# Optimization experiments

Hardware: AMD Instinct MI355X
Metric: run time of the kernel (lower is better)

The kernel has to match this reference:

```python
import jax, jax.numpy as jnp
import numpy as np

HEAD_SIZE = 64


def setup_inputs() -> dict:
    key = jax.random.key(0)
    kx, kq, kk, kv = jax.random.split(key, 4)
    B, L, D = 4, 4096, 1024
    scale = 1.0 / np.sqrt(D)
    x = jax.random.normal(kx, (B, L, D), dtype=jnp.float32)
    Wq = jax.random.normal(kq, (D, HEAD_SIZE), dtype=jnp.float32) * scale
    Wk = jax.random.normal(kk, (D, HEAD_SIZE), dtype=jnp.float32) * scale
    Wv = jax.random.normal(kv, (D, HEAD_SIZE), dtype=jnp.float32) * scale
    return {"x": x, "Wq": Wq, "Wk": Wk, "Wv": Wv}


def reference(x, Wq, Wk, Wv):
    B, L, D = x.shape
    H = Wq.shape[1]
    q = jnp.einsum('bld,dh->blh', x, Wq)  # [B,L,H]
    k = jnp.einsum('bld,dh->blh', x, Wk)
    v = jnp.einsum('bld,dh->blh', x, Wv)
    # full L x L score matrix, as in the original module
    scores = jnp.einsum('bqh,bkh->bqk', q, k) / jnp.sqrt(jnp.float32(H))
    causal = jnp.tril(jnp.ones((L, L), dtype=bool))
    scores = jnp.where(causal, scores, -jnp.inf)
    attn = jax.nn.softmax(scores, axis=-1)
    z = jnp.einsum('bqk,bkh->bqh', attn, v)  # [B,L,H]
    return z
```

## Files before the change

kernel.cpp:

```cpp
#include <hip/hip_runtime.h>
#include <stdint.h>

#define L_SEQ 4096
#define D_MODEL 1024
#define HEAD 64
#define CHUNK 512
#define MAXCH 8

typedef unsigned short u16;
typedef __attribute__((ext_vector_type(8))) short bf16x8;
typedef __attribute__((ext_vector_type(4))) float f32x4;

static __device__ __forceinline__ u16 f2bf(float f) {
    union { float f; uint32_t u; } c; c.f = f;
    uint32_t u = c.u;
    return (u16)((u + 0x7FFFu + ((u >> 16) & 1u)) >> 16);
}
static __device__ __forceinline__ bf16x8 ld8(const u16* p) { return *(const bf16x8*)p; }

static __device__ __forceinline__ f32x4 mfma16(bf16x8 a, bf16x8 b, f32x4 c) {
    return __builtin_amdgcn_mfma_f32_16x16x32_bf16(a, b, c, 0, 0, 0);
}

__global__ __launch_bounds__(256) void conv_w(
    const float* __restrict__ Wq, const float* __restrict__ Wk,
    const float* __restrict__ Wv, u16* __restrict__ Wt)
{
    __shared__ u16 tile[64][72];
    const float* W = (blockIdx.y == 0) ? Wq : (blockIdx.y == 1) ? Wk : Wv;
    u16* dst = Wt + blockIdx.y * (HEAD * D_MODEL);
    const int k0 = blockIdx.x * 64, t = threadIdx.x;
    #pragma unroll
    for (int i = 0; i < 16; i++) {
        int idx = i * 256 + t;
        int kk = idx >> 6, h = idx & 63;
        tile[h][kk] = f2bf(W[(size_t)(k0 + kk) * HEAD + h]);
    }
    __syncthreads();
    #pragma unroll
    for (int i = 0; i < 16; i++) {
        int idx = i * 256 + t;
        int h = idx >> 6, kk = idx & 63;
        dst[(size_t)h * D_MODEL + k0 + kk] = tile[h][kk];
    }
}

__global__ __launch_bounds__(256) void qkv_proj(
    const float* __restrict__ x, const u16* __restrict__ Wt,
    u16* __restrict__ qb, u16* __restrict__ kb, u16* __restrict__ vTb)
{
    __shared__ __align__(16) char smem[64512];
    u16* WlB = (u16*)smem;
    u16* XlB = (u16*)(smem + 55296);
    u16* CtB = (u16*)smem;
#define WL(bb,r,c) WlB[((bb)*192 + (r))*72 + (c)]
#define XL(bb,r,c) XlB[((bb)*32  + (r))*72 + (c)]
#define CT(r,c)    CtB[(r)*200 + (c)]

    const int t = threadIdx.x;
    const int wv = t >> 6, lane = t & 63;
    const int ln16 = lane & 15, quad = lane >> 4;
    const int w3 = wv * 3;
    const int m0 = blockIdx.x * 32;

    f32x4 acc[2][3] = {};

    auto stage = [&](int s, int bb) {
        const int k0 = s * 64;
        #pragma unroll
        for (int i = 0; i < 6; i++) {
            int idx = i * 256 + t;
            int row = idx >> 3, cg = (idx & 7) * 8;
            bf16x8 wv8 = ld8(&Wt[(size_t)row * D_MODEL + k0 + cg]);
            *(bf16x8*)&WL(bb, row, cg) = wv8;
        }
        #pragma unroll
        for (int i = 0; i < 2; i++) {
            int idx = i * 256 + t;
            int row = idx >> 4, cs = (idx & 15) * 4;
            const float4 xv = *(const float4*)&x[(size_t)(m0 + row) * D_MODEL + k0 + cs];
            uint2 pk;
            pk.x = (uint32_t)f2bf(xv.x) | ((uint32_t)f2bf(xv.y) << 16);
            pk.y = (uint32_t)f2bf(xv.z) | ((uint32_t)f2bf(xv.w) << 16);
            *(uint2*)&XL(bb, row, cs) = pk;
        }
    };

    stage(0, 0);
    int buf = 0;
    for (int s = 0; s < 16; s++) {
        __syncthreads();
        if (s + 1 < 16) stage(s + 1, buf ^ 1);
        #pragma unroll
        for (int c = 0; c < 2; c++) {
            bf16x8 xb0 = ld8(&XL(buf, ln16,      c * 32 + quad * 8));
            bf16x8 xb1 = ld8(&XL(buf, 16 + ln16, c * 32 + quad * 8));
            #pragma unroll
            for (int j = 0; j < 3; j++) {
                bf16x8 af = ld8(&WL(buf, (w3 + j) * 16 + ln16, c * 32 + quad * 8));
                acc[0][j] = mfma16(af, xb0, acc[0][j]);
                acc[1][j] = mfma16(af, xb1, acc[1][j]);
            }
        }
        buf ^= 1;
    }

    __syncthreads();
    #pragma unroll
    for (int mt = 0; mt < 2; mt++) {
        #pragma unroll
        for (int j = 0; j < 3; j++) {
            int g0 = (w3 + j) * 16 + quad * 4;
            float sc = (g0 < 64) ? 0.125f : 1.0f;
            uint2 pk;
            pk.x = (uint32_t)f2bf(acc[mt][j][0] * sc) | ((uint32_t)f2bf(acc[mt][j][1] * sc) << 16);
            pk.y = (uint32_t)f2bf(acc[mt][j][2] * sc) | ((uint32_t)f2bf(acc[mt][j][3] * sc) << 16);
            *(uint2*)&CT(mt * 16 + ln16, g0) = pk;
        }
    }
    __syncthreads();
    {
        int m = t >> 3, hg = (t & 7) * 8;
        *(bf16x8*)&qb[(size_t)(m0 + m) * HEAD + hg] = *(bf16x8*)&CT(m, hg);
        *(bf16x8*)&kb[(size_t)(m0 + m) * HEAD + hg] = *(bf16x8*)&CT(m, 64 + hg);
        int h = t >> 2, mg = (t & 3) * 8;
        bf16x8 vv;
        #pragma unroll
        for (int jj = 0; jj < 8; jj++) vv[jj] = (short)CT(mg + jj, 128 + h);
        int bbt = m0 >> 12, l0 = m0 & 4095;
        *(bf16x8*)&vTb[(size_t)(bbt * HEAD + h) * L_SEQ + l0 + mg] = vv;
    }
#undef WL
#undef XL
#undef CT
}

__global__ __launch_bounds__(256) void attn_chunk(
    const u16* __restrict__ qb, const u16* __restrict__ kb,
    const u16* __restrict__ vT, float* __restrict__ Opart, float* __restrict__ lpart)
{
    const int qt = blockIdx.x, ch = blockIdx.y, b = blockIdx.z;
    if (ch * CHUNK > qt * 64 + 63) return;

    __shared__ __align__(16) char smem[18432];

    const int t = threadIdx.x, wv = t >> 6, lane = t & 63;
    const int ln16 = lane & 15, quad = lane >> 4;
    const int qh = wv & 1, kvh = wv >> 1;
    const int qmin0 = qt * 64 + qh * 32;

    u16 (*P)[72] = (u16(*)[72])smem + wv * 32;
    float (*Cb)[68] = (float(*)[68])smem;
    float* Lb = (float*)(smem + 17408);

    bf16x8 qf[2][2];
    #pragma unroll
    for (int qn = 0; qn < 2; qn++) {
        const u16* qrp = qb + (size_t)(b * L_SEQ + qmin0 + qn * 16 + ln16) * HEAD + quad * 8;
        qf[qn][0] = ld8(qrp); qf[qn][1] = ld8(qrp + 32);
    }

    const u16* kbb = kb + (size_t)b * L_SEQ * HEAD;
    const u16* vbb = vT + (size_t)b * HEAD * L_SEQ;

    f32x4 o[2][4] = {};
    float lsum[2] = {0.f, 0.f};

    const int kv_lo = ch * CHUNK + kvh * (CHUNK / 2);
    const int kv_hi = min(kv_lo + CHUNK / 2, qt * 64 + 64);

    bf16x8 kf0a, kf0b, kf1a, kf1b;
    if (kv_lo < kv_hi) {
        const u16* kr0 = kbb + (size_t)(kv_lo + ln16) * HEAD + quad * 8;
        kf0a = ld8(kr0); kf0b = ld8(kr0 + 32);
        const u16* kr1 = kbb + (size_t)(kv_lo + 16 + ln16) * HEAD + quad * 8;
        kf1a = ld8(kr1); kf1b = ld8(kr1 + 32);
    }

    for (int kv0 = kv_lo; kv0 < kv_hi; kv0 += 64) {
        const u16* kr2 = kbb + (size_t)(kv0 + 32 + ln16) * HEAD + quad * 8;
        bf16x8 kf2a = ld8(kr2), kf2b = ld8(kr2 + 32);
        const u16* kr3 = kbb + (size_t)(kv0 + 48 + ln16) * HEAD + quad * 8;
        bf16x8 kf3a = ld8(kr3), kf3b = ld8(kr3 + 32);
        int kv0n = (kv0 + 64 < kv_hi) ? kv0 + 64 : kv_lo;
        const u16* nr0 = kbb + (size_t)(kv0n + ln16) * HEAD + quad * 8;
        bf16x8 nk0a = ld8(nr0), nk0b = ld8(nr0 + 32);
        const u16* nr1 = kbb + (size_t)(kv0n + 16 + ln16) * HEAD + quad * 8;
        bf16x8 nk1a = ld8(nr1), nk1b = ld8(nr1 + 32);
        const u16* vr0 = vbb + (size_t)ln16 * L_SEQ + kv0 + quad * 8;
        bf16x8 vf0a = ld8(vr0), vf0b = ld8(vr0 + 32);
        const u16* vr1 = vbb + (size_t)(16 + ln16) * L_SEQ + kv0 + quad * 8;
        bf16x8 vf1a = ld8(vr1), vf1b = ld8(vr1 + 32);

        #pragma unroll
        for (int g = 0; g < 4; g++) {
            bf16x8 ka = (g == 0) ? kf0a : (g == 1) ? kf1a : (g == 2) ? kf2a : kf3a;
            bf16x8 kb8 = (g == 0) ? kf0b : (g == 1) ? kf1b : (g == 2) ? kf2b : kf3b;
            #pragma unroll
            for (int qn = 0; qn < 2; qn++) {
                f32x4 s = {};
                s = mfma16(ka, qf[qn][0], s);
                s = mfma16(kb8, qf[qn][1], s);
                float p0, p1, p2, p3;
                if (kv0 + g * 16 + 15 <= qmin0 + qn * 16) {
                    p0 = __expf(s[0]); p1 = __expf(s[1]);
                    p2 = __expf(s[2]); p3 = __expf(s[3]);
                } else {
                    int q = qmin0 + qn * 16 + ln16;
                    int kv = kv0 + g * 16 + quad * 4;
                    p0 = (kv     <= q) ? __expf(s[0]) : 0.f;
                    p1 = (kv + 1 <= q) ? __expf(s[1]) : 0.f;
                    p2 = (kv + 2 <= q) ? __expf(s[2]) : 0.f;
                    p3 = (kv + 3 <= q) ? __expf(s[3]) : 0.f;
                }
                lsum[qn] += p0 + p1 + p2 + p3;
                uint32_t lo = (uint32_t)f2bf(p0) | ((uint32_t)f2bf(p1) << 16);
                uint32_t hi = (uint32_t)f2bf(p2) | ((uint32_t)f2bf(p3) << 16);
                uint32_t* dst = (uint32_t*)&P[qn * 16 + ln16][g * 16 + quad * 4];
                dst[0] = lo; dst[1] = hi;
            }
        }
        bf16x8 pf0[2], pf1[2];
        #pragma unroll
        for (int qn = 0; qn < 2; qn++) {
            pf0[qn] = ld8(&P[qn * 16 + ln16][quad * 8]);
            pf1[qn] = ld8(&P[qn * 16 + ln16][32 + quad * 8]);
        }
        #pragma unroll
        for (int hg = 0; hg < 4; hg++) {
            bf16x8 va, vb2;
            if (hg == 0) { va = vf0a; vb2 = vf0b; }
            else if (hg == 1) { va = vf1a; vb2 = vf1b; }
            else {
                const u16* vr = vbb + (size_t)(hg * 16 + ln16) * L_SEQ + kv0 + quad * 8;
                va = ld8(vr); vb2 = ld8(vr + 32);
            }
            #pragma unroll
            for (int qn = 0; qn < 2; qn++) {
                o[qn][hg] = mfma16(va, pf0[qn], o[qn][hg]);
                o[qn][hg] = mfma16(vb2, pf1[qn], o[qn][hg]);
            }
        }
        kf0a = nk0a; kf0b = nk0b; kf1a = nk1a; kf1b = nk1b;
    }

    #pragma unroll
    for (int qn = 0; qn < 2; qn++) {
        lsum[qn] += __shfl_xor(lsum[qn], 16);
        lsum[qn] += __shfl_xor(lsum[qn], 32);
    }

    __syncthreads();
    if (kvh == 1) {
        #pragma unroll
        for (int qn = 0; qn < 2; qn++) {
            #pragma unroll
            for (int hg = 0; hg < 4; hg++)
                *(f32x4*)&Cb[qh * 32 + qn * 16 + ln16][hg * 16 + quad * 4] = o[qn][hg];
            if (quad == 0) Lb[qh * 32 + qn * 16 + ln16] = lsum[qn];
        }
    }
    __syncthreads();
    if (kvh == 0) {
        const size_t base = (size_t)((b * 64 + qt) * MAXCH + ch);
        #pragma unroll
        for (int qn = 0; qn < 2; qn++) {
            int qrow = qh * 32 + qn * 16 + ln16;
            #pragma unroll
            for (int hg = 0; hg < 4; hg++) {
                f32x4 other = *(f32x4*)&Cb[qrow][hg * 16 + quad * 4];
                f32x4 r = o[qn][hg];
                r[0] += other[0]; r[1] += other[1]; r[2] += other[2]; r[3] += other[3];
                *(f32x4*)&Opart[base * 4096 + (size_t)qrow * 64 + hg * 16 + quad * 4] = r;
            }
            if (quad == 0)
                lpart[base * 64 + qrow] = lsum[qn] + Lb[qrow];
        }
    }
}

__global__ __launch_bounds__(256) void merge_chunks(
    const float* __restrict__ Opart, const float* __restrict__ lpart,
    float* __restrict__ out)
{
    const int qt = blockIdx.x, b = blockIdx.y;
    const int nch = qt / 8 + 1;
    const int t = threadIdx.x;
    const size_t obase = (size_t)((b * 64 + qt) * MAXCH) * 4096;
    const size_t lbase = (size_t)((b * 64 + qt) * MAXCH) * 64;
    #pragma unroll
    for (int i = 0; i < 4; i++) {
        int idx = i * 256 + t;
        int q = idx >> 4, hg = (idx & 15) * 4;
        float L = 0.f;
        float ax = 0.f, ay = 0.f, az = 0.f, aw = 0.f;
        for (int c = 0; c < nch; c++) {
            L += lpart[lbase + c * 64 + q];
            const float4 v = *(const float4*)&Opart[obase + (size_t)c * 4096 + q * 64 + hg];
            ax += v.x; ay += v.y; az += v.z; aw += v.w;
        }
        float inv = 1.f / L;
        float4 r; r.x = ax * inv; r.y = ay * inv; r.z = az * inv; r.w = aw * inv;
        *(float4*)&out[((size_t)(b * L_SEQ + qt * 64 + q)) * HEAD + hg] = r;
    }
}

extern "C" void kernel_launch(void* const* d_in, const int* in_sizes, int n_in,
                              void* d_out, int out_size, void* d_ws, size_t ws_size,
                              hipStream_t stream) {
    const float* x  = (const float*)d_in[0];
    const float* Wq = (const float*)d_in[1];
    const float* Wk = (const float*)d_in[2];
    const float* Wv = (const float*)d_in[3];
    float* out = (float*)d_out;

    u16* ws16 = (u16*)d_ws;
    u16* Wt  = ws16;
    u16* qb  = Wt + 3 * HEAD * D_MODEL;
    u16* kb  = qb + 16384 * HEAD;
    u16* vTb = kb + 16384 * HEAD;
    float* Opart = (float*)(vTb + 16384 * HEAD);
    float* lpart = Opart + (size_t)2048 * 4096;

    conv_w      <<<dim3(16, 3), 256, 0, stream>>>(Wq, Wk, Wv, Wt);
    qkv_proj    <<<dim3(512), 256, 0, stream>>>(x, Wt, qb, kb, vTb);
    attn_chunk  <<<dim3(64, 8, 4), 256, 0, stream>>>(qb, kb, vTb, Opart, lpart);
    merge_chunks<<<dim3(64, 4), 256, 0, stream>>>(Opart, lpart, out);
}
```

Measured before the change: 175.5 us.

## Split attention into 32-row query tiles with four KV-split waves and preloaded K/V

Query tiles shrink from 64 to 32 rows, doubling the grid, and the four waves in a block now each take a 128-key slice of the chunk instead of a 2x2 query/KV split. All K and V fragments for a wave's two 64-key tiles are loaded up front, and the partial results are reduced across waves through shared memory. The merge kernel loads all chunk partials unconditionally and masks them. The aim is more blocks and better load balance across the causal triangle, plus more latency hiding from bulk loads, at the cost of higher register pressure, a larger LDS footprint and more partial-result traffic.

```diff
diff --git a/kernel.cpp b/kernel.cpp
--- a/kernel.cpp
+++ b/kernel.cpp
@@ -6,6 +6,7 @@
 #define HEAD 64
 #define CHUNK 512
 #define MAXCH 8
+#define NQT 128
 
 typedef unsigned short u16;
 typedef __attribute__((ext_vector_type(8))) short bf16x8;
@@ -135,23 +136,20 @@
 #undef CT
 }
 
-__global__ __launch_bounds__(256) void attn_chunk(
+__global__ __launch_bounds__(256, 2) void attn_chunk(
     const u16* __restrict__ qb, const u16* __restrict__ kb,
     const u16* __restrict__ vT, float* __restrict__ Opart, float* __restrict__ lpart)
 {
     const int qt = blockIdx.x, ch = blockIdx.y, b = blockIdx.z;
-    if (ch * CHUNK > qt * 64 + 63) return;
-
-    __shared__ __align__(16) char smem[18432];
+    if (ch * CHUNK > qt * 32 + 31) return;
+
+    __shared__ __align__(16) char smem[26496];
 
     const int t = threadIdx.x, wv = t >> 6, lane = t & 63;
     const int ln16 = lane & 15, quad = lane >> 4;
-    const int qh = wv & 1, kvh = wv >> 1;
-    const int qmin0 = qt * 64 + qh * 32;
+    const int qmin0 = qt * 32;
 
     u16 (*P)[72] = (u16(*)[72])smem + wv * 32;
-    float (*Cb)[68] = (float(*)[68])smem;
-    float* Lb = (float*)(smem + 17408);
 
     bf16x8 qf[2][2];
     #pragma unroll
@@ -166,41 +164,42 @@
     f32x4 o[2][4] = {};
     float lsum[2] = {0.f, 0.f};
 
-    const int kv_lo = ch * CHUNK + kvh * (CHUNK / 2);
-    const int kv_hi = min(kv_lo + CHUNK / 2, qt * 64 + 64);
-
-    bf16x8 kf0a, kf0b, kf1a, kf1b;
-    if (kv_lo < kv_hi) {
-        const u16* kr0 = kbb + (size_t)(kv_lo + ln16) * HEAD + quad * 8;
-        kf0a = ld8(kr0); kf0b = ld8(kr0 + 32);
-        const u16* kr1 = kbb + (size_t)(kv_lo + 16 + ln16) * HEAD + quad * 8;
-        kf1a = ld8(kr1); kf1b = ld8(kr1 + 32);
-    }
-
-    for (int kv0 = kv_lo; kv0 < kv_hi; kv0 += 64) {
-        const u16* kr2 = kbb + (size_t)(kv0 + 32 + ln16) * HEAD + quad * 8;
-        bf16x8 kf2a = ld8(kr2), kf2b = ld8(kr2 + 32);
-        const u16* kr3 = kbb + (size_t)(kv0 + 48 + ln16) * HEAD + quad * 8;
-        bf16x8 kf3a = ld8(kr3), kf3b = ld8(kr3 + 32);
-        int kv0n = (kv0 + 64 < kv_hi) ? kv0 + 64 : kv_lo;
-        const u16* nr0 = kbb + (size_t)(kv0n + ln16) * HEAD + quad * 8;
-        bf16x8 nk0a = ld8(nr0), nk0b = ld8(nr0 + 32);
-        const u16* nr1 = kbb + (size_t)(kv0n + 16 + ln16) * HEAD + quad * 8;
-        bf16x8 nk1a = ld8(nr1), nk1b = ld8(nr1 + 32);
-        const u16* vr0 = vbb + (size_t)ln16 * L_SEQ + kv0 + quad * 8;
-        bf16x8 vf0a = ld8(vr0), vf0b = ld8(vr0 + 32);
-        const u16* vr1 = vbb + (size_t)(16 + ln16) * L_SEQ + kv0 + quad * 8;
-        bf16x8 vf1a = ld8(vr1), vf1b = ld8(vr1 + 32);
-
+    const int blk_hi = min(ch * CHUNK + CHUNK, qt * 32 + 32);
+    const int kv_lo = ch * CHUNK + wv * 128;
+    const int kv_hi = min(kv_lo + 128, blk_hi);
+    const bool has0 = kv_lo < kv_hi;
+    const bool has1 = kv_lo + 64 < kv_hi;
+
+    bf16x8 K0a[4], K0b[4], V0a[4], V0b[4];
+    bf16x8 K1a[4], K1b[4], V1a[4], V1b[4];
+
+    if (has0) {
         #pragma unroll
         for (int g = 0; g < 4; g++) {
-            bf16x8 ka = (g == 0) ? kf0a : (g == 1) ? kf1a : (g == 2) ? kf2a : kf3a;
-            bf16x8 kb8 = (g == 0) ? kf0b : (g == 1) ? kf1b : (g == 2) ? kf2b : kf3b;
+            const u16* kr = kbb + (size_t)(kv_lo + g * 16 + ln16) * HEAD + quad * 8;
+            K0a[g] = ld8(kr); K0b[g] = ld8(kr + 32);
+            const u16* vr = vbb + (size_t)(g * 16 + ln16) * L_SEQ + kv_lo + quad * 8;
+            V0a[g] = ld8(vr); V0b[g] = ld8(vr + 32);
+        }
+    }
+    if (has1) {
+        #pragma unroll
+        for (int g = 0; g < 4; g++) {
+            const u16* kr = kbb + (size_t)(kv_lo + 64 + g * 16 + ln16) * HEAD + quad * 8;
+            K1a[g] = ld8(kr); K1b[g] = ld8(kr + 32);
+            const u16* vr = vbb + (size_t)(g * 16 + ln16) * L_SEQ + kv_lo + 64 + quad * 8;
+            V1a[g] = ld8(vr); V1b[g] = ld8(vr + 32);
+        }
+    }
+
+    auto tile = [&](int kv0, bf16x8* Ka, bf16x8* Kb2, bf16x8* Va, bf16x8* Vb2) {
+        #pragma unroll
+        for (int g = 0; g < 4; g++) {
             #pragma unroll
             for (int qn = 0; qn < 2; qn++) {
                 f32x4 s = {};
-                s = mfma16(ka, qf[qn][0], s);
-                s = mfma16(kb8, qf[qn][1], s);
+                s = mfma16(Ka[g], qf[qn][0], s);
+                s = mfma16(Kb2[g], qf[qn][1], s);
                 float p0, p1, p2, p3;
                 if (kv0 + g * 16 + 15 <= qmin0 + qn * 16) {
                     p0 = __expf(s[0]); p1 = __expf(s[1]);
@@ -228,21 +227,16 @@
         }
         #pragma unroll
         for (int hg = 0; hg < 4; hg++) {
-            bf16x8 va, vb2;
-            if (hg == 0) { va = vf0a; vb2 = vf0b; }
-            else if (hg == 1) { va = vf1a; vb2 = vf1b; }
-            else {
-                const u16* vr = vbb + (size_t)(hg * 16 + ln16) * L_SEQ + kv0 + quad * 8;
-                va = ld8(vr); vb2 = ld8(vr + 32);
+            #pragma unroll
+            for (int qn = 0; qn < 2; qn++) {
+                o[qn][hg] = mfma16(Va[hg], pf0[qn], o[qn][hg]);
+                o[qn][hg] = mfma16(Vb2[hg], pf1[qn], o[qn][hg]);
             }
-            #pragma unroll
-            for (int qn = 0; qn < 2; qn++) {
-                o[qn][hg] = mfma16(va, pf0[qn], o[qn][hg]);
-                o[qn][hg] = mfma16(vb2, pf1[qn], o[qn][hg]);
-            }
-        }
-        kf0a = nk0a; kf0b = nk0b; kf1a = nk1a; kf1b = nk1b;
-    }
+        }
+    };
+
+    if (has0) tile(kv_lo,      K0a, K0b, V0a, V0b);
+    if (has1) tile(kv_lo + 64, K1a, K1b, V1a, V1b);
 
     #pragma unroll
     for (int qn = 0; qn < 2; qn++) {
@@ -251,30 +245,38 @@
     }
 
     __syncthreads();
-    if (kvh == 1) {
+    float (*cb)[68] = (float(*)[68])smem;
+    float* lb = (float*)(smem + 26112);
+    if (wv > 0) {
         #pragma unroll
         for (int qn = 0; qn < 2; qn++) {
             #pragma unroll
             for (int hg = 0; hg < 4; hg++)
-                *(f32x4*)&Cb[qh * 32 + qn * 16 + ln16][hg * 16 + quad * 4] = o[qn][hg];
-            if (quad == 0) Lb[qh * 32 + qn * 16 + ln16] = lsum[qn];
-        }
-    }
-    __syncthreads();
-    if (kvh == 0) {
-        const size_t base = (size_t)((b * 64 + qt) * MAXCH + ch);
+                *(f32x4*)&cb[(wv - 1) * 32 + qn * 16 + ln16][hg * 16 + quad * 4] = o[qn][hg];
+            if (quad == 0) lb[(wv - 1) * 32 + qn * 16 + ln16] = lsum[qn];
+        }
+    }
+    __syncthreads();
+    if (wv == 0) {
+        const size_t base = (size_t)((b * NQT + qt) * MAXCH + ch);
         #pragma unroll
         for (int qn = 0; qn < 2; qn++) {
-            int qrow = qh * 32 + qn * 16 + ln16;
-            #pragma unroll
-            for (int hg = 0; hg < 4; hg++) {
-                f32x4 other = *(f32x4*)&Cb[qrow][hg * 16 + quad * 4];
-                f32x4 r = o[qn][hg];
-                r[0] += other[0]; r[1] += other[1]; r[2] += other[2]; r[3] += other[3];
-                *(f32x4*)&Opart[base * 4096 + (size_t)qrow * 64 + hg * 16 + quad * 4] = r;
+            int q = qn * 16 + ln16;
+            #pragma unroll
+            for (int w2 = 0; w2 < 3; w2++) {
+                lsum[qn] += lb[w2 * 32 + q];
+                #pragma unroll
+                for (int hg = 0; hg < 4; hg++) {
+                    f32x4 v = *(f32x4*)&cb[w2 * 32 + q][hg * 16 + quad * 4];
+                    o[qn][hg][0] += v[0]; o[qn][hg][1] += v[1];
+                    o[qn][hg][2] += v[2]; o[qn][hg][3] += v[3];
+                }
             }
+            #pragma unroll
+            for (int hg = 0; hg < 4; hg++)
+                *(f32x4*)&Opart[base * 2048 + (size_t)q * 64 + hg * 16 + quad * 4] = o[qn][hg];
             if (quad == 0)
-                lpart[base * 64 + qrow] = lsum[qn] + Lb[qrow];
+                lpart[base * 32 + q] = lsum[qn];
         }
     }
 }
@@ -284,24 +286,32 @@
     float* __restrict__ out)
 {
     const int qt = blockIdx.x, b = blockIdx.y;
-    const int nch = qt / 8 + 1;
+    const int nch = qt / 16 + 1;
     const int t = threadIdx.x;
-    const size_t obase = (size_t)((b * 64 + qt) * MAXCH) * 4096;
-    const size_t lbase = (size_t)((b * 64 + qt) * MAXCH) * 64;
-    #pragma unroll
-    for (int i = 0; i < 4; i++) {
+    const size_t obase = (size_t)((b * NQT + qt) * MAXCH) * 2048;
+    const size_t lbase = (size_t)((b * NQT + qt) * MAXCH) * 32;
+    #pragma unroll
+    for (int i = 0; i < 2; i++) {
         int idx = i * 256 + t;
         int q = idx >> 4, hg = (idx & 15) * 4;
-        float L = 0.f;
-        float ax = 0.f, ay = 0.f, az = 0.f, aw = 0.f;
-        for (int c = 0; c < nch; c++) {
-            L += lpart[lbase + c * 64 + q];
-            const float4 v = *(const float4*)&Opart[obase + (size_t)c * 4096 + q * 64 + hg];
-            ax += v.x; ay += v.y; az += v.z; aw += v.w;
+        f32x4 vals[MAXCH];
+        float ls[MAXCH];
+        #pragma unroll
+        for (int c = 0; c < MAXCH; c++) {
+            vals[c] = *(const f32x4*)&Opart[obase + (size_t)c * 2048 + q * 64 + hg];
+            ls[c] = lpart[lbase + c * 32 + q];
+        }
+        float L = 0.f, ax = 0.f, ay = 0.f, az = 0.f, aw = 0.f;
+        #pragma unroll
+        for (int c = 0; c < MAXCH; c++) {
+            float m = (c < nch) ? 1.f : 0.f;
+            L += ls[c] * m;
+            ax += vals[c][0] * m; ay += vals[c][1] * m;
+            az += vals[c][2] * m; aw += vals[c][3] * m;
         }
         float inv = 1.f / L;
         float4 r; r.x = ax * inv; r.y = ay * inv; r.z = az * inv; r.w = aw * inv;
-        *(float4*)&out[((size_t)(b * L_SEQ + qt * 64 + q)) * HEAD + hg] = r;
+        *(float4*)&out[((size_t)(b * L_SEQ + qt * 32 + q)) * HEAD + hg] = r;
     }
 }
 
@@ -320,10 +330,10 @@
     u16* kb  = qb + 16384 * HEAD;
     u16* vTb = kb + 16384 * HEAD;
     float* Opart = (float*)(vTb + 16384 * HEAD);
-    float* lpart = Opart + (size_t)2048 * 4096;
+    float* lpart = Opart + (size_t)4096 * 2048;
 
     conv_w      <<<dim3(16, 3), 256, 0, stream>>>(Wq, Wk, Wv, Wt);
     qkv_proj    <<<dim3(512), 256, 0, stream>>>(x, Wt, qb, kb, vTb);
-    attn_chunk  <<<dim3(64, 8, 4), 256, 0, stream>>>(qb, kb, vTb, Opart, lpart);
-    merge_chunks<<<dim3(64, 4), 256, 0, stream>>>(Opart, lpart, out);
-}
+    attn_chunk  <<<dim3(NQT, 8, 4), 256, 0, stream>>>(qb, kb, vTb, Opart, lpart);
+    merge_chunks<<<dim3(NQT, 4), 256, 0, stream>>>(Opart, lpart, out);
+}
```

Result: faster. 168.4 us (-4.0%).
